# Performance work log

Hardware: AMD Instinct MI355X
Metric: run time of the kernel (lower is better)

Reference implementation:

```python
import jax, jax.numpy as jnp
import numpy as np
import math

H = 16          # num_attention_heads
D = 64          # attention_head_size
MAX_POS = 1024  # max_position_embeddings


def setup_inputs() -> dict:
    key = jax.random.key(0)
    ks = jax.random.split(key, 8)
    B, S, E = 4, 1024, 1024
    return {
        "hidden_states": jax.random.normal(ks[0], (B, S, E), jnp.float32),
        "wq": jax.random.normal(ks[1], (E, E), jnp.float32) * 0.02,
        "bq": jax.random.normal(ks[2], (E,), jnp.float32) * 0.02,
        "wk": jax.random.normal(ks[3], (E, E), jnp.float32) * 0.02,
        "bk": jax.random.normal(ks[4], (E,), jnp.float32) * 0.02,
        "wv": jax.random.normal(ks[5], (E, E), jnp.float32) * 0.02,
        "bv": jax.random.normal(ks[6], (E,), jnp.float32) * 0.02,
        "dist_emb": jax.random.normal(ks[7], (2 * MAX_POS - 1, D), jnp.float32) * 0.02,
    }


def reference(hidden_states, wq, bq, wk, bk, wv, bv, dist_emb):
    B, S, E = hidden_states.shape

    def proj(w, b):
        # nn.Linear: x @ W^T + b, then split heads -> [B, H, S, D]
        y = jnp.einsum("bse,fe->bsf", hidden_states, w) + b
        return y.reshape(B, S, H, D).transpose(0, 2, 1, 3)

    q = proj(wq, bq)
    k = proj(wk, bk)
    v = proj(wv, bv)

    # raw attention scores [B, H, S, S]
    scores = jnp.einsum("bhld,bhrd->bhlr", q, k)

    # relative_key_query positional bias
    pos = jnp.arange(S)
    distance = pos[:, None] - pos[None, :] + (MAX_POS - 1)  # [S, S]
    pe = dist_emb[distance]  # [S, S, D]
    scores = scores \
        + jnp.einsum("bhld,lrd->bhlr", q, pe) \
        + jnp.einsum("bhrd,lrd->bhlr", k, pe)

    scores = scores / math.sqrt(D)
    probs = jax.nn.softmax(scores, axis=-1)  # dropout p=0 -> identity

    ctx = jnp.einsum("bhlr,bhrd->bhld", probs, v)
    ctx = ctx.transpose(0, 2, 1, 3).reshape(B, S, H * D)
    return ctx
```

## Files before the change

kernel.cpp:

```cpp
#include <hip/hip_runtime.h>

typedef __attribute__((ext_vector_type(8))) short bf16x8;
typedef __attribute__((ext_vector_type(4))) float f32x4;
typedef __attribute__((ext_vector_type(4))) unsigned short u16x4;
typedef __attribute__((ext_vector_type(8))) unsigned short u16x8;

namespace {
constexpr size_t OFF_Q = 0;
constexpr size_t OFF_K = 4194304;
constexpr size_t OFF_VT = 8388608;
constexpr size_t OFF_DB = 12582912;
constexpr size_t OFF_XB = 12713920;
constexpr size_t OFF_WB = 16908224;
}

__device__ __forceinline__ unsigned short f2bf(float f) {
  union { float f; unsigned u; } v; v.f = f;
  unsigned r = v.u + 0x7FFFu + ((v.u >> 16) & 1u);
  return (unsigned short)(r >> 16);
}
__device__ __forceinline__ float bf2f(unsigned short h) {
  union { unsigned u; float f; } v; v.u = ((unsigned)h) << 16;
  return v.f;
}

__global__ __launch_bounds__(256) void cvt_all(
    const float* __restrict__ X, const float* __restrict__ Wq,
    const float* __restrict__ Wk, const float* __restrict__ Wv,
    const float* __restrict__ De, unsigned short* __restrict__ ws) {
  const int z = blockIdx.y;
  const float* src = z == 0 ? X : z == 1 ? Wq : z == 2 ? Wk : z == 3 ? Wv : De;
  unsigned short* dst = z == 0 ? ws + OFF_XB
                      : z == 4 ? ws + OFF_DB
                               : ws + OFF_WB + (size_t)(z - 1) * 1048576;
  const int n = z == 0 ? 4194304 : z == 4 ? 131008 : 1048576;
  const int idx = (blockIdx.x * 256 + threadIdx.x) * 8;
  if (idx < n) {
    const float4 f0 = *(const float4*)(src + idx);
    const float4 f1 = *(const float4*)(src + idx + 4);
    u16x8 o;
    o[0] = f2bf(f0.x); o[1] = f2bf(f0.y); o[2] = f2bf(f0.z); o[3] = f2bf(f0.w);
    o[4] = f2bf(f1.x); o[5] = f2bf(f1.y); o[6] = f2bf(f1.z); o[7] = f2bf(f1.w);
    *(u16x8*)(dst + idx) = o;
  }
}

__global__ __launch_bounds__(256) void proj2(
    const unsigned short* __restrict__ Xb, const unsigned short* __restrict__ Wb3,
    const float* __restrict__ Bq, const float* __restrict__ Bk,
    const float* __restrict__ Bv, unsigned short* __restrict__ qo,
    unsigned short* __restrict__ ko, unsigned short* __restrict__ vto) {
  __shared__ unsigned short As[128 * 72];
  __shared__ unsigned short Bs[128 * 72];
  const int which = blockIdx.z;
  const unsigned short* W = Wb3 + (size_t)which * 1048576;
  const float* bias = which == 0 ? Bq : which == 1 ? Bk : Bv;
  const int m0 = blockIdx.x * 128, n0 = blockIdx.y * 128;
  const int tid = threadIdx.x;
  const int wid = tid >> 6, lane = tid & 63;
  const int lrow = lane & 15, lgrp = lane >> 4;
  const int wr0 = (wid >> 1) * 64, wc0 = (wid & 1) * 64;
  const int srow = tid >> 1, scol = (tid & 1) * 32;

  f32x4 acc[4][4] = {};
  for (int k0 = 0; k0 < 1024; k0 += 64) {
    u16x8 a[4], bb[4];
    const unsigned short* Ap = Xb + (size_t)(m0 + srow) * 1024 + k0 + scol;
    const unsigned short* Bp = W + (size_t)(n0 + srow) * 1024 + k0 + scol;
#pragma unroll
    for (int j = 0; j < 4; ++j) {
      a[j] = *(const u16x8*)(Ap + j * 8);
      bb[j] = *(const u16x8*)(Bp + j * 8);
    }
    __syncthreads();
#pragma unroll
    for (int j = 0; j < 4; ++j) {
      *(u16x8*)&As[srow * 72 + scol + j * 8] = a[j];
      *(u16x8*)&Bs[srow * 72 + scol + j * 8] = bb[j];
    }
    __syncthreads();
#pragma unroll
    for (int ks = 0; ks < 2; ++ks) {
      bf16x8 af[4], bfr[4];
#pragma unroll
      for (int rb = 0; rb < 4; ++rb)
        af[rb] = *(const bf16x8*)&As[(wr0 + rb * 16 + lrow) * 72 + ks * 32 + lgrp * 8];
#pragma unroll
      for (int cb = 0; cb < 4; ++cb)
        bfr[cb] = *(const bf16x8*)&Bs[(wc0 + cb * 16 + lrow) * 72 + ks * 32 + lgrp * 8];
#pragma unroll
      for (int rb = 0; rb < 4; ++rb)
#pragma unroll
        for (int cb = 0; cb < 4; ++cb)
          acc[rb][cb] = __builtin_amdgcn_mfma_f32_16x16x32_bf16(af[rb], bfr[cb], acc[rb][cb], 0, 0, 0);
    }
  }
  if (which < 2) {
    unsigned short* dst = (which == 0) ? qo : ko;
#pragma unroll
    for (int cb = 0; cb < 4; ++cb) {
      const int n = n0 + wc0 + cb * 16 + lrow;
      const float bval = bias[n];
      const int h = n >> 6, d = n & 63;
#pragma unroll
      for (int rb = 0; rb < 4; ++rb)
#pragma unroll
        for (int reg = 0; reg < 4; ++reg) {
          const int m = m0 + wr0 + rb * 16 + lgrp * 4 + reg;
          const int b_ = m >> 10, s_ = m & 1023;
          dst[(((size_t)(b_ * 16 + h) * 1024 + s_) << 6) | d] = f2bf(acc[rb][cb][reg] + bval);
        }
    }
  } else {
#pragma unroll
    for (int cb = 0; cb < 4; ++cb) {
      const int n = n0 + wc0 + cb * 16 + lrow;
      const float bval = bias[n];
      const int h = n >> 6, d = n & 63;
#pragma unroll
      for (int rb = 0; rb < 4; ++rb) {
        const int mb = m0 + wr0 + rb * 16 + lgrp * 4;
        const int b_ = mb >> 10, s_ = mb & 1023;
        u16x4 o;
#pragma unroll
        for (int reg = 0; reg < 4; ++reg) o[reg] = f2bf(acc[rb][cb][reg] + bval);
        *(u16x4*)(vto + ((size_t)(b_ * 16 + h) * 64 + d) * 1024 + s_) = o;
      }
    }
  }
}

__global__ __launch_bounds__(512, 4) void attn8(
    const unsigned short* __restrict__ Qg, const unsigned short* __restrict__ Kg,
    const unsigned short* __restrict__ Vtg, const unsigned short* __restrict__ PEg,
    float* __restrict__ out) {
  __shared__ unsigned short Ks[64 * 72];
  __shared__ unsigned short Vts[64 * 72];
  __shared__ unsigned short PEs[128 * 72];
  __shared__ unsigned short Ub[64 * 84];
  __shared__ unsigned short Wb[64 * 84];
  __shared__ unsigned short Ps[64 * 72];
  __shared__ float red[2][2][64];

  const int bh = blockIdx.x;
  const int l0 = blockIdx.y * 64;
  const int b = bh >> 4, h = bh & 15;
  const int tid = threadIdx.x;
  const int wid = tid >> 6, lane = tid & 63;
  const int lrow = lane & 15, lgrp = lane >> 4;
  const int qr = wid >> 1, ch = wid & 1;
  const bool isU = wid < 4;
  const int us = isU ? wid : wid - 4;

  {
    const int row = tid >> 3, c0 = (tid & 7) * 8;
    *(u16x8*)&Ps[row * 72 + c0] = *(const u16x8*)(Qg + ((size_t)bh * 1024 + l0 + row) * 64 + c0);
  }
  __syncthreads();
  bf16x8 qaS[2], qaU[2];
#pragma unroll
  for (int ks = 0; ks < 2; ++ks)
    qaS[ks] = *(const bf16x8*)&Ps[(qr * 16 + lrow) * 72 + ks * 32 + lgrp * 8];
  if (isU) {
#pragma unroll
    for (int ks = 0; ks < 2; ++ks)
      qaU[ks] = *(const bf16x8*)&Ps[(us * 16 + lrow) * 72 + ks * 32 + lgrp * 8];
  }

  float m[4], den[4];
#pragma unroll
  for (int r = 0; r < 4; ++r) { m[r] = -1e30f; den[r] = 0.f; }
  f32x4 acc[2] = {};

  for (int t = 0; t < 16; ++t) {
    const int r0 = t * 64;
    __syncthreads();
    {
      const int row = tid >> 3, c0 = (tid & 7) * 8;
      *(u16x8*)&Ks[row * 72 + c0] = *(const u16x8*)(Kg + ((size_t)bh * 1024 + r0 + row) * 64 + c0);
      *(u16x8*)&Vts[row * 72 + c0] = *(const u16x8*)(Vtg + ((size_t)bh * 64 + row) * 1024 + r0 + c0);
      const int prow = tid >> 2, pc0 = (tid & 3) * 16;
      if (prow < 127) {
        const unsigned short* psrc = PEg + (size_t)(l0 - r0 + 960 + prow) * 64 + pc0;
        *(u16x8*)&PEs[prow * 72 + pc0] = *(const u16x8*)psrc;
        *(u16x8*)&PEs[prow * 72 + pc0 + 8] = *(const u16x8*)(psrc + 8);
      } else {
        const u16x8 zz = {0, 0, 0, 0, 0, 0, 0, 0};
        *(u16x8*)&PEs[prow * 72 + pc0] = zz;
        *(u16x8*)&PEs[prow * 72 + pc0 + 8] = zz;
      }
    }
    __syncthreads();

    f32x4 uw[5] = {};
    const int pebase = isU ? us * 16 : 48 - us * 16;
    bf16x8 aUW[2];
    if (isU) { aUW[0] = qaU[0]; aUW[1] = qaU[1]; }
    else {
#pragma unroll
      for (int ks = 0; ks < 2; ++ks)
        aUW[ks] = *(const bf16x8*)&Ks[(us * 16 + lrow) * 72 + ks * 32 + lgrp * 8];
    }
#pragma unroll
    for (int ks = 0; ks < 2; ++ks)
#pragma unroll
      for (int cb = 0; cb < 5; ++cb) {
        const bf16x8 pb = *(const bf16x8*)&PEs[(pebase + cb * 16 + lrow) * 72 + ks * 32 + lgrp * 8];
        uw[cb] = __builtin_amdgcn_mfma_f32_16x16x32_bf16(aUW[ks], pb, uw[cb], 0, 0, 0);
      }
    {
      unsigned short* buf = isU ? Ub : Wb;
#pragma unroll
      for (int cb = 0; cb < 5; ++cb)
#pragma unroll
        for (int reg = 0; reg < 4; ++reg)
          buf[(us * 16 + lgrp * 4 + reg) * 84 + cb * 16 + lrow] = f2bf(uw[cb][reg]);
    }
    f32x4 sc[2] = {};
#pragma unroll
    for (int ks = 0; ks < 2; ++ks)
#pragma unroll
      for (int cb = 0; cb < 2; ++cb) {
        const bf16x8 kb = *(const bf16x8*)&Ks[(ch * 32 + cb * 16 + lrow) * 72 + ks * 32 + lgrp * 8];
        sc[cb] = __builtin_amdgcn_mfma_f32_16x16x32_bf16(qaS[ks], kb, sc[cb], 0, 0, 0);
      }
    __syncthreads();

#pragma unroll
    for (int cb = 0; cb < 2; ++cb)
#pragma unroll
      for (int reg = 0; reg < 4; ++reg) {
        const int l = qr * 16 + lgrp * 4 + reg;
        const int r = ch * 32 + cb * 16 + lrow;
        const float uu = bf2f(Ub[l * 84 + (l & 15) - r + 63]);
        const float ww = bf2f(Wb[r * 84 + l - (r & 15) + 15]);
        sc[cb][reg] = (sc[cb][reg] + uu + ww) * 0.125f;
      }
    float rmax[4];
#pragma unroll
    for (int reg = 0; reg < 4; ++reg) {
      rmax[reg] = fmaxf(sc[0][reg], sc[1][reg]);
      rmax[reg] = fmaxf(rmax[reg], __shfl_xor(rmax[reg], 1));
      rmax[reg] = fmaxf(rmax[reg], __shfl_xor(rmax[reg], 2));
      rmax[reg] = fmaxf(rmax[reg], __shfl_xor(rmax[reg], 4));
      rmax[reg] = fmaxf(rmax[reg], __shfl_xor(rmax[reg], 8));
    }
    if (lrow == 0) {
#pragma unroll
      for (int reg = 0; reg < 4; ++reg) red[0][ch][qr * 16 + lgrp * 4 + reg] = rmax[reg];
    }
    __syncthreads();
    float fr[4], psum[4];
#pragma unroll
    for (int reg = 0; reg < 4; ++reg) {
      const int l = qr * 16 + lgrp * 4 + reg;
      const float jm = fmaxf(red[0][0][l], red[0][1][l]);
      const float mn = fmaxf(m[reg], jm);
      fr[reg] = __expf(m[reg] - mn);
      m[reg] = mn;
      psum[reg] = 0.f;
    }
#pragma unroll
    for (int cb = 0; cb < 2; ++cb)
#pragma unroll
      for (int reg = 0; reg < 4; ++reg) {
        const float p = __expf(sc[cb][reg] - m[reg]);
        Ps[(qr * 16 + lgrp * 4 + reg) * 72 + ch * 32 + cb * 16 + lrow] = f2bf(p);
        psum[reg] += p;
      }
#pragma unroll
    for (int reg = 0; reg < 4; ++reg) {
      psum[reg] += __shfl_xor(psum[reg], 1);
      psum[reg] += __shfl_xor(psum[reg], 2);
      psum[reg] += __shfl_xor(psum[reg], 4);
      psum[reg] += __shfl_xor(psum[reg], 8);
    }
    if (lrow == 0) {
#pragma unroll
      for (int reg = 0; reg < 4; ++reg) red[1][ch][qr * 16 + lgrp * 4 + reg] = psum[reg];
    }
    __syncthreads();
#pragma unroll
    for (int reg = 0; reg < 4; ++reg) {
      const int l = qr * 16 + lgrp * 4 + reg;
      den[reg] = den[reg] * fr[reg] + red[1][0][l] + red[1][1][l];
    }
#pragma unroll
    for (int cb = 0; cb < 2; ++cb)
#pragma unroll
      for (int reg = 0; reg < 4; ++reg) acc[cb][reg] *= fr[reg];
#pragma unroll
    for (int ks = 0; ks < 2; ++ks) {
      const bf16x8 pa = *(const bf16x8*)&Ps[(qr * 16 + lrow) * 72 + ks * 32 + lgrp * 8];
#pragma unroll
      for (int cb = 0; cb < 2; ++cb) {
        const bf16x8 vb = *(const bf16x8*)&Vts[(ch * 32 + cb * 16 + lrow) * 72 + ks * 32 + lgrp * 8];
        acc[cb] = __builtin_amdgcn_mfma_f32_16x16x32_bf16(pa, vb, acc[cb], 0, 0, 0);
      }
    }
  }

#pragma unroll
  for (int cb = 0; cb < 2; ++cb)
#pragma unroll
    for (int reg = 0; reg < 4; ++reg) {
      const int l = qr * 16 + lgrp * 4 + reg;
      const int d = ch * 32 + cb * 16 + lrow;
      out[((size_t)b * 1024 + l0 + l) * 1024 + h * 64 + d] = acc[cb][reg] / den[reg];
    }
}

extern "C" void kernel_launch(void* const* d_in, const int* in_sizes, int n_in,
                              void* d_out, int out_size, void* d_ws, size_t ws_size,
                              hipStream_t stream) {
  const float* hs = (const float*)d_in[0];
  const float* wq = (const float*)d_in[1];
  const float* bq = (const float*)d_in[2];
  const float* wk = (const float*)d_in[3];
  const float* bk = (const float*)d_in[4];
  const float* wv = (const float*)d_in[5];
  const float* bv = (const float*)d_in[6];
  const float* de = (const float*)d_in[7];

  unsigned short* wsb = (unsigned short*)d_ws;
  unsigned short* q = wsb + OFF_Q;
  unsigned short* k = wsb + OFF_K;
  unsigned short* vt = wsb + OFF_VT;
  unsigned short* db = wsb + OFF_DB;
  unsigned short* xb = wsb + OFF_XB;
  unsigned short* wb3 = wsb + OFF_WB;

  cvt_all<<<dim3(2048, 5), 256, 0, stream>>>(hs, wq, wk, wv, de, wsb);
  proj2<<<dim3(32, 8, 3), 256, 0, stream>>>(xb, wb3, bq, bk, bv, q, k, vt);
  attn8<<<dim3(64, 16), 512, 0, stream>>>(q, k, vt, db, (float*)d_out);
}
```

Baseline: 310.9 us.

## Warp-specialize attention kernel with register-prefetched producer warps

Splits the 512-thread block into four consumer warps, each owning 16 query rows, and four producer warps. Producers compute the key-side positional bias and prefetch the next K/V/PE tile into registers while consumers run QK, the query-side bias, softmax and PV. Each consumer now holds whole rows, so the block-wide max and sum reductions through shared memory and two barriers per tile go away. The kernel also uses packed bf16 conversion and vectorized float4 output stores, at the cost of half the warps doing no MFMA work for the main matmuls.

Measured after the change: 285.9 us. -8.1%, faster.

```diff
diff --git a/kernel.cpp b/kernel.cpp
--- a/kernel.cpp
+++ b/kernel.cpp
@@ -22,6 +22,11 @@
 __device__ __forceinline__ float bf2f(unsigned short h) {
   union { unsigned u; float f; } v; v.u = ((unsigned)h) << 16;
   return v.f;
+}
+__device__ __forceinline__ unsigned cvtpk(float lo, float hi) {
+  unsigned r;
+  asm("v_cvt_pk_bf16_f32 %0, %1, %2" : "=v"(r) : "v"(lo), "v"(hi));
+  return r;
 }
 
 __global__ __launch_bounds__(256) void cvt_all(
@@ -130,17 +135,37 @@
   }
 }
 
-__global__ __launch_bounds__(512, 4) void attn8(
+struct StageRegs { u16x8 k[2]; u16x8 v[2]; u16x8 pe[4]; };
+
+__device__ __forceinline__ void issue_loads(
+    StageRegs& R, const unsigned short* Kg, const unsigned short* Vtg,
+    const unsigned short* PEg, int bh, int l0, int r0, int pt) {
+#pragma unroll
+  for (int i = 0; i < 2; ++i) {
+    const int cc = pt + 256 * i, row = cc >> 3, col = (cc & 7) * 8;
+    R.k[i] = *(const u16x8*)(Kg + ((size_t)bh * 1024 + r0 + row) * 64 + col);
+    R.v[i] = *(const u16x8*)(Vtg + ((size_t)bh * 64 + row) * 1024 + r0 + col);
+  }
+#pragma unroll
+  for (int i = 0; i < 4; ++i) {
+    const int cc = pt + 256 * i, row = cc >> 3, col = (cc & 7) * 8;
+    if (row < 127)
+      R.pe[i] = *(const u16x8*)(PEg + (size_t)(l0 - r0 + 960 + row) * 64 + col);
+    else
+      R.pe[i] = (u16x8){0, 0, 0, 0, 0, 0, 0, 0};
+  }
+}
+
+__global__ __launch_bounds__(512, 4) void attn_ws(
     const unsigned short* __restrict__ Qg, const unsigned short* __restrict__ Kg,
     const unsigned short* __restrict__ Vtg, const unsigned short* __restrict__ PEg,
     float* __restrict__ out) {
   __shared__ unsigned short Ks[64 * 72];
   __shared__ unsigned short Vts[64 * 72];
   __shared__ unsigned short PEs[128 * 72];
-  __shared__ unsigned short Ub[64 * 84];
-  __shared__ unsigned short Wb[64 * 84];
-  __shared__ unsigned short Ps[64 * 72];
-  __shared__ float red[2][2][64];
+  __shared__ unsigned short Ws[64 * 84];
+  __shared__ unsigned short QUs[4 * 1408];
+  __shared__ unsigned short Ps[4 * 1152];
 
   const int bh = blockIdx.x;
   const int l0 = blockIdx.y * 64;
@@ -148,166 +173,162 @@
   const int tid = threadIdx.x;
   const int wid = tid >> 6, lane = tid & 63;
   const int lrow = lane & 15, lgrp = lane >> 4;
-  const int qr = wid >> 1, ch = wid & 1;
-  const bool isU = wid < 4;
-  const int us = isU ? wid : wid - 4;
-
-  {
-    const int row = tid >> 3, c0 = (tid & 7) * 8;
-    *(u16x8*)&Ps[row * 72 + c0] = *(const u16x8*)(Qg + ((size_t)bh * 1024 + l0 + row) * 64 + c0);
+  const bool prod = wid >= 4;
+  const int us = wid - 4;
+  const int pt = (us << 6) | lane;
+
+  StageRegs R;
+  if (prod) {
+    issue_loads(R, Kg, Vtg, PEg, bh, l0, 0, pt);
+  } else {
+    const int c0 = (wid << 6) | lane;
+#pragma unroll
+    for (int i = 0; i < 2; ++i) {
+      const int cc = c0 + 256 * i, row = cc >> 3, col = (cc & 7) * 8;
+      *(u16x8*)&QUs[(row >> 4) * 1408 + (row & 15) * 88 + col] =
+          *(const u16x8*)(Qg + ((size_t)bh * 1024 + l0 + row) * 64 + col);
+    }
   }
   __syncthreads();
-  bf16x8 qaS[2], qaU[2];
-#pragma unroll
-  for (int ks = 0; ks < 2; ++ks)
-    qaS[ks] = *(const bf16x8*)&Ps[(qr * 16 + lrow) * 72 + ks * 32 + lgrp * 8];
-  if (isU) {
+  bf16x8 qB[2];
+  if (!prod) {
 #pragma unroll
     for (int ks = 0; ks < 2; ++ks)
-      qaU[ks] = *(const bf16x8*)&Ps[(us * 16 + lrow) * 72 + ks * 32 + lgrp * 8];
-  }
-
-  float m[4], den[4];
-#pragma unroll
-  for (int r = 0; r < 4; ++r) { m[r] = -1e30f; den[r] = 0.f; }
-  f32x4 acc[2] = {};
+      qB[ks] = *(const bf16x8*)&QUs[wid * 1408 + lrow * 88 + ks * 32 + lgrp * 8];
+  }
+
+  float mrun = -1e30f, den = 0.f;
+  f32x4 acc[4] = {};
 
   for (int t = 0; t < 16; ++t) {
-    const int r0 = t * 64;
-    __syncthreads();
-    {
-      const int row = tid >> 3, c0 = (tid & 7) * 8;
-      *(u16x8*)&Ks[row * 72 + c0] = *(const u16x8*)(Kg + ((size_t)bh * 1024 + r0 + row) * 64 + c0);
-      *(u16x8*)&Vts[row * 72 + c0] = *(const u16x8*)(Vtg + ((size_t)bh * 64 + row) * 1024 + r0 + c0);
-      const int prow = tid >> 2, pc0 = (tid & 3) * 16;
-      if (prow < 127) {
-        const unsigned short* psrc = PEg + (size_t)(l0 - r0 + 960 + prow) * 64 + pc0;
-        *(u16x8*)&PEs[prow * 72 + pc0] = *(const u16x8*)psrc;
-        *(u16x8*)&PEs[prow * 72 + pc0 + 8] = *(const u16x8*)(psrc + 8);
-      } else {
-        const u16x8 zz = {0, 0, 0, 0, 0, 0, 0, 0};
-        *(u16x8*)&PEs[prow * 72 + pc0] = zz;
-        *(u16x8*)&PEs[prow * 72 + pc0 + 8] = zz;
-      }
-    }
-    __syncthreads();
-
-    f32x4 uw[5] = {};
-    const int pebase = isU ? us * 16 : 48 - us * 16;
-    bf16x8 aUW[2];
-    if (isU) { aUW[0] = qaU[0]; aUW[1] = qaU[1]; }
-    else {
+    const int r0 = t << 6;
+    __syncthreads();
+    if (prod) {
+#pragma unroll
+      for (int i = 0; i < 2; ++i) {
+        const int cc = pt + 256 * i, row = cc >> 3, col = (cc & 7) * 8;
+        *(u16x8*)&Ks[row * 72 + col] = R.k[i];
+        *(u16x8*)&Vts[row * 72 + col] = R.v[i];
+      }
+#pragma unroll
+      for (int i = 0; i < 4; ++i) {
+        const int cc = pt + 256 * i, row = cc >> 3, col = (cc & 7) * 8;
+        *(u16x8*)&PEs[row * 72 + col] = R.pe[i];
+      }
+    }
+    __syncthreads();
+
+    f32x4 sc[4];
+    if (!prod) {
+#pragma unroll
+      for (int cb = 0; cb < 5; ++cb) {
+        f32x4 u = {0.f, 0.f, 0.f, 0.f};
+#pragma unroll
+        for (int ks = 0; ks < 2; ++ks) {
+          const bf16x8 pe = *(const bf16x8*)&PEs[(wid * 16 + cb * 16 + lrow) * 72 + ks * 32 + lgrp * 8];
+          u = __builtin_amdgcn_mfma_f32_16x16x32_bf16(pe, qB[ks], u, 0, 0, 0);
+        }
+        const int ubase = wid * 1408 + lrow * 88 + cb * 16 + lgrp * 4;
+        *(unsigned*)&QUs[ubase] = cvtpk(u[0], u[1]);
+        *(unsigned*)&QUs[ubase + 2] = cvtpk(u[2], u[3]);
+      }
+#pragma unroll
+      for (int cb = 0; cb < 4; ++cb) sc[cb] = (f32x4){0.f, 0.f, 0.f, 0.f};
 #pragma unroll
       for (int ks = 0; ks < 2; ++ks)
-        aUW[ks] = *(const bf16x8*)&Ks[(us * 16 + lrow) * 72 + ks * 32 + lgrp * 8];
-    }
-#pragma unroll
-    for (int ks = 0; ks < 2; ++ks)
+#pragma unroll
+        for (int cb = 0; cb < 4; ++cb) {
+          const bf16x8 kf = *(const bf16x8*)&Ks[(cb * 16 + lrow) * 72 + ks * 32 + lgrp * 8];
+          sc[cb] = __builtin_amdgcn_mfma_f32_16x16x32_bf16(kf, qB[ks], sc[cb], 0, 0, 0);
+        }
+    } else {
+      bf16x8 kB[2];
+#pragma unroll
+      for (int ks = 0; ks < 2; ++ks)
+        kB[ks] = *(const bf16x8*)&Ks[(us * 16 + lrow) * 72 + ks * 32 + lgrp * 8];
+      const int peb = 48 - us * 16;
 #pragma unroll
       for (int cb = 0; cb < 5; ++cb) {
-        const bf16x8 pb = *(const bf16x8*)&PEs[(pebase + cb * 16 + lrow) * 72 + ks * 32 + lgrp * 8];
-        uw[cb] = __builtin_amdgcn_mfma_f32_16x16x32_bf16(aUW[ks], pb, uw[cb], 0, 0, 0);
-      }
-    {
-      unsigned short* buf = isU ? Ub : Wb;
-#pragma unroll
-      for (int cb = 0; cb < 5; ++cb)
-#pragma unroll
-        for (int reg = 0; reg < 4; ++reg)
-          buf[(us * 16 + lgrp * 4 + reg) * 84 + cb * 16 + lrow] = f2bf(uw[cb][reg]);
-    }
-    f32x4 sc[2] = {};
-#pragma unroll
-    for (int ks = 0; ks < 2; ++ks)
-#pragma unroll
-      for (int cb = 0; cb < 2; ++cb) {
-        const bf16x8 kb = *(const bf16x8*)&Ks[(ch * 32 + cb * 16 + lrow) * 72 + ks * 32 + lgrp * 8];
-        sc[cb] = __builtin_amdgcn_mfma_f32_16x16x32_bf16(qaS[ks], kb, sc[cb], 0, 0, 0);
-      }
-    __syncthreads();
-
-#pragma unroll
-    for (int cb = 0; cb < 2; ++cb)
-#pragma unroll
-      for (int reg = 0; reg < 4; ++reg) {
-        const int l = qr * 16 + lgrp * 4 + reg;
-        const int r = ch * 32 + cb * 16 + lrow;
-        const float uu = bf2f(Ub[l * 84 + (l & 15) - r + 63]);
-        const float ww = bf2f(Wb[r * 84 + l - (r & 15) + 15]);
-        sc[cb][reg] = (sc[cb][reg] + uu + ww) * 0.125f;
-      }
-    float rmax[4];
-#pragma unroll
-    for (int reg = 0; reg < 4; ++reg) {
-      rmax[reg] = fmaxf(sc[0][reg], sc[1][reg]);
-      rmax[reg] = fmaxf(rmax[reg], __shfl_xor(rmax[reg], 1));
-      rmax[reg] = fmaxf(rmax[reg], __shfl_xor(rmax[reg], 2));
-      rmax[reg] = fmaxf(rmax[reg], __shfl_xor(rmax[reg], 4));
-      rmax[reg] = fmaxf(rmax[reg], __shfl_xor(rmax[reg], 8));
-    }
-    if (lrow == 0) {
-#pragma unroll
-      for (int reg = 0; reg < 4; ++reg) red[0][ch][qr * 16 + lgrp * 4 + reg] = rmax[reg];
-    }
-    __syncthreads();
-    float fr[4], psum[4];
-#pragma unroll
-    for (int reg = 0; reg < 4; ++reg) {
-      const int l = qr * 16 + lgrp * 4 + reg;
-      const float jm = fmaxf(red[0][0][l], red[0][1][l]);
-      const float mn = fmaxf(m[reg], jm);
-      fr[reg] = __expf(m[reg] - mn);
-      m[reg] = mn;
-      psum[reg] = 0.f;
-    }
-#pragma unroll
-    for (int cb = 0; cb < 2; ++cb)
-#pragma unroll
-      for (int reg = 0; reg < 4; ++reg) {
-        const float p = __expf(sc[cb][reg] - m[reg]);
-        Ps[(qr * 16 + lgrp * 4 + reg) * 72 + ch * 32 + cb * 16 + lrow] = f2bf(p);
-        psum[reg] += p;
-      }
-#pragma unroll
-    for (int reg = 0; reg < 4; ++reg) {
-      psum[reg] += __shfl_xor(psum[reg], 1);
-      psum[reg] += __shfl_xor(psum[reg], 2);
-      psum[reg] += __shfl_xor(psum[reg], 4);
-      psum[reg] += __shfl_xor(psum[reg], 8);
-    }
-    if (lrow == 0) {
-#pragma unroll
-      for (int reg = 0; reg < 4; ++reg) red[1][ch][qr * 16 + lgrp * 4 + reg] = psum[reg];
-    }
-    __syncthreads();
-#pragma unroll
-    for (int reg = 0; reg < 4; ++reg) {
-      const int l = qr * 16 + lgrp * 4 + reg;
-      den[reg] = den[reg] * fr[reg] + red[1][0][l] + red[1][1][l];
-    }
-#pragma unroll
-    for (int cb = 0; cb < 2; ++cb)
-#pragma unroll
-      for (int reg = 0; reg < 4; ++reg) acc[cb][reg] *= fr[reg];
-#pragma unroll
-    for (int ks = 0; ks < 2; ++ks) {
-      const bf16x8 pa = *(const bf16x8*)&Ps[(qr * 16 + lrow) * 72 + ks * 32 + lgrp * 8];
-#pragma unroll
-      for (int cb = 0; cb < 2; ++cb) {
-        const bf16x8 vb = *(const bf16x8*)&Vts[(ch * 32 + cb * 16 + lrow) * 72 + ks * 32 + lgrp * 8];
-        acc[cb] = __builtin_amdgcn_mfma_f32_16x16x32_bf16(pa, vb, acc[cb], 0, 0, 0);
-      }
-    }
-  }
-
-#pragma unroll
-  for (int cb = 0; cb < 2; ++cb)
-#pragma unroll
-    for (int reg = 0; reg < 4; ++reg) {
-      const int l = qr * 16 + lgrp * 4 + reg;
-      const int d = ch * 32 + cb * 16 + lrow;
-      out[((size_t)b * 1024 + l0 + l) * 1024 + h * 64 + d] = acc[cb][reg] / den[reg];
-    }
+        f32x4 w = {0.f, 0.f, 0.f, 0.f};
+#pragma unroll
+        for (int ks = 0; ks < 2; ++ks) {
+          const bf16x8 pe = *(const bf16x8*)&PEs[(peb + cb * 16 + lrow) * 72 + ks * 32 + lgrp * 8];
+          w = __builtin_amdgcn_mfma_f32_16x16x32_bf16(pe, kB[ks], w, 0, 0, 0);
+        }
+        const int wbase = (us * 16 + lrow) * 84 + cb * 16 + lgrp * 4;
+        *(unsigned*)&Ws[wbase] = cvtpk(w[0], w[1]);
+        *(unsigned*)&Ws[wbase + 2] = cvtpk(w[2], w[3]);
+      }
+      if (t < 15) issue_loads(R, Kg, Vtg, PEg, bh, l0, r0 + 64, pt);
+    }
+    __syncthreads();
+
+    if (!prod) {
+      const int ub = wid * 1408 + lrow * 89 + 63;
+#pragma unroll
+      for (int cb = 0; cb < 4; ++cb)
+#pragma unroll
+        for (int reg = 0; reg < 4; ++reg) {
+          const int r = cb * 16 + lgrp * 4 + reg;
+          const float uu = bf2f(QUs[ub - r]);
+          const float ww = bf2f(Ws[r * 84 + lrow + 15 - lgrp * 4 - reg]);
+          sc[cb][reg] = (sc[cb][reg] + uu + ww) * 0.125f;
+        }
+      float tmax = -1e30f;
+#pragma unroll
+      for (int cb = 0; cb < 4; ++cb)
+#pragma unroll
+        for (int reg = 0; reg < 4; ++reg) tmax = fmaxf(tmax, sc[cb][reg]);
+      tmax = fmaxf(tmax, __shfl_xor(tmax, 16));
+      tmax = fmaxf(tmax, __shfl_xor(tmax, 32));
+      const float mn = fmaxf(mrun, tmax);
+      const float fr = __expf(mrun - mn);
+      mrun = mn;
+      float psum = 0.f;
+#pragma unroll
+      for (int cb = 0; cb < 4; ++cb)
+#pragma unroll
+        for (int reg = 0; reg < 4; ++reg) {
+          const float p = __expf(sc[cb][reg] - mn);
+          sc[cb][reg] = p;
+          psum += p;
+        }
+      psum += __shfl_xor(psum, 16);
+      psum += __shfl_xor(psum, 32);
+      den = den * fr + psum;
+#pragma unroll
+      for (int cb = 0; cb < 4; ++cb) {
+        const int pb = wid * 1152 + lrow * 72 + cb * 16 + lgrp * 4;
+        *(unsigned*)&Ps[pb] = cvtpk(sc[cb][0], sc[cb][1]);
+        *(unsigned*)&Ps[pb + 2] = cvtpk(sc[cb][2], sc[cb][3]);
+      }
+#pragma unroll
+      for (int cb = 0; cb < 4; ++cb)
+#pragma unroll
+        for (int reg = 0; reg < 4; ++reg) acc[cb][reg] *= fr;
+#pragma unroll
+      for (int ks = 0; ks < 2; ++ks) {
+        const bf16x8 pB = *(const bf16x8*)&Ps[wid * 1152 + lrow * 72 + ks * 32 + lgrp * 8];
+#pragma unroll
+        for (int cb = 0; cb < 4; ++cb) {
+          const bf16x8 vA = *(const bf16x8*)&Vts[(cb * 16 + lrow) * 72 + ks * 32 + lgrp * 8];
+          acc[cb] = __builtin_amdgcn_mfma_f32_16x16x32_bf16(vA, pB, acc[cb], 0, 0, 0);
+        }
+      }
+    }
+  }
+
+  if (!prod) {
+    const float inv = 1.f / den;
+    float* orow = out + ((size_t)b * 1024 + l0 + wid * 16 + lrow) * 1024 + h * 64;
+#pragma unroll
+    for (int cb = 0; cb < 4; ++cb) {
+      float4 o;
+      o.x = acc[cb][0] * inv; o.y = acc[cb][1] * inv;
+      o.z = acc[cb][2] * inv; o.w = acc[cb][3] * inv;
+      *(float4*)(orow + cb * 16 + lgrp * 4) = o;
+    }
+  }
 }
 
 extern "C" void kernel_launch(void* const* d_in, const int* in_sizes, int n_in,
@@ -332,5 +353,5 @@
 
   cvt_all<<<dim3(2048, 5), 256, 0, stream>>>(hs, wq, wk, wv, de, wsb);
   proj2<<<dim3(32, 8, 3), 256, 0, stream>>>(xb, wb3, bq, bk, bv, q, k, vt);
-  attn8<<<dim3(64, 16), 512, 0, stream>>>(q, k, vt, db, (float*)d_out);
-}
+  attn_ws<<<dim3(64, 16), 512, 0, stream>>>(q, k, vt, db, (float*)d_out);
+}
```
